# Optimization experiments

Hardware: AMD Instinct MI355X
Metric: run time of the kernel (lower is better)

The kernel has to match this reference:

```python
import jax, jax.numpy as jnp
import numpy as np

B, S_IMG, S_TXT, S_BOK = 1, 2048, 512, 4
DM, H, DH, R = 3072, 24, 128, 16
LORA_SCALE, LORA_ALPHA, BOKEH_SCALE = 1.0, 16.0, 1.0
EPS = 1e-6


def _rms_norm(x, w):
    # normalize over head_dim (last axis), Flux RMSNorm eps=1e-6
    var = jnp.mean(jnp.square(x), axis=-1, keepdims=True)
    return x * jax.lax.rsqrt(var + EPS) * w


def _lora(x, w_down, w_up):
    # LoRALinear: up(down(x)) * alpha/rank
    return (x @ w_down.T) @ w_up.T * (LORA_ALPHA / R)


def _apply_rope(x, cos, sin):
    # x: [B,H,S,D]; cos/sin: [S,D]; diffusers use_real=True, unbind_dim=-1 (interleaved pairs)
    x1 = x[..., 0::2]
    x2 = x[..., 1::2]
    rot = jnp.stack([-x2, x1], axis=-1).reshape(x.shape)
    return x * cos[None, None] + rot * sin[None, None]


def _sdpa(q, k, v):
    # q:[B,H,Sq,D] k,v:[B,H,Sk,D]
    scale = 1.0 / jnp.sqrt(jnp.asarray(q.shape[-1], q.dtype))
    scores = jnp.einsum('bhqd,bhkd->bhqk', q, k) * scale
    p = jax.nn.softmax(scores, axis=-1)
    return jnp.einsum('bhqk,bhkd->bhqd', p, v)


def setup_inputs() -> dict:
    key = jax.random.key(0)
    ks = jax.random.split(key, 40)
    std = 0.02
    d = {}
    d['hidden_states'] = jax.random.normal(ks[0], (B, S_IMG, DM), jnp.float32)
    d['encoder_hidden_states'] = jax.random.normal(ks[1], (B, S_TXT, DM), jnp.float32)
    d['bokeh_embeds'] = jax.random.normal(ks[2], (B, S_BOK, DM), jnp.float32)
    theta = jax.random.uniform(ks[3], (S_TXT + S_IMG, DH // 2), jnp.float32) * 2 * np.pi
    theta = jnp.repeat(theta, 2, axis=-1)  # interleaved pairs share angle
    d['rope_cos'] = jnp.cos(theta)
    d['rope_sin'] = jnp.sin(theta)
    # base attention params
    for i, nm in enumerate(['Wq', 'Wk', 'Wv', 'Waq', 'Wak', 'Wav', 'Wo', 'Wao']):
        d[nm] = jax.random.normal(ks[4 + i], (DM, DM), jnp.float32) * std
    for i, nm in enumerate(['bq', 'bk', 'bv', 'baq', 'bak', 'bav', 'bo', 'bao']):
        d[nm] = jax.random.normal(ks[12 + i], (DM,), jnp.float32) * std
    for i, nm in enumerate(['norm_q_w', 'norm_k_w', 'norm_aq_w', 'norm_ak_w']):
        d[nm] = 1.0 + jax.random.normal(ks[20 + i], (DH,), jnp.float32) * std
    # LoRA adapters (up weights random, not zero, for nontrivial math)
    for i, nm in enumerate(['kb_down', 'vb_down', 'qadp_down', 'kadp_down']):
        d[nm] = jax.random.normal(ks[24 + i], (R, DM), jnp.float32) * (1.0 / R)
    for i, nm in enumerate(['kb_up', 'vb_up', 'qadp_up', 'kadp_up']):
        d[nm] = jax.random.normal(ks[28 + i], (DM, R), jnp.float32) * std
    return d


def reference(hidden_states, encoder_hidden_states, bokeh_embeds, rope_cos, rope_sin,
              Wq, Wk, Wv, Waq, Wak, Wav, Wo, Wao,
              bq, bk, bv, baq, bak, bav, bo, bao,
              norm_q_w, norm_k_w, norm_aq_w, norm_ak_w,
              kb_down, vb_down, qadp_down, kadp_down,
              kb_up, vb_up, qadp_up, kadp_up):
    Bsz = encoder_hidden_states.shape[0]

    def heads(x):  # [B,S,DM] -> [B,H,S,DH]
        return x.reshape(Bsz, -1, H, DH).transpose(0, 2, 1, 3)

    q = hidden_states @ Wq.T + bq
    k = hidden_states @ Wk.T + bk
    v = hidden_states @ Wv.T + bv
    q = q + LORA_SCALE * _lora(q, qadp_down, qadp_up)
    k = k + LORA_SCALE * _lora(k, kadp_down, kadp_up)
    q, k, v = heads(q), heads(k), heads(v)
    q = _rms_norm(q, norm_q_w)
    k = _rms_norm(k, norm_k_w)

    eq = heads(encoder_hidden_states @ Waq.T + baq)
    ek = heads(encoder_hidden_states @ Wak.T + bak)
    ev = heads(encoder_hidden_states @ Wav.T + bav)
    eq = _rms_norm(eq, norm_aq_w)
    ek = _rms_norm(ek, norm_ak_w)

    q = jnp.concatenate([eq, q], axis=2)
    k = jnp.concatenate([ek, k], axis=2)
    v = jnp.concatenate([ev, v], axis=2)

    q = _apply_rope(q, rope_cos, rope_sin)
    k = _apply_rope(k, rope_cos, rope_sin)

    out = _sdpa(q, k, v)  # [B,H,S,DH]
    out = out.transpose(0, 2, 1, 3).reshape(Bsz, -1, H * DH)

    # bokeh pass
    kd = heads(_lora(bokeh_embeds, kb_down, kb_up))
    vd = heads(_lora(bokeh_embeds, vb_down, vb_up))
    cam = _sdpa(q, kd, vd).transpose(0, 2, 1, 3).reshape(Bsz, -1, H * DH)
    out = out + BOKEH_SCALE * cam

    enc_out = out[:, :S_TXT]
    img_out = out[:, S_TXT:]
    img_out = img_out @ Wo.T + bo
    enc_out = enc_out @ Wao.T + bao
    return (img_out, enc_out)
```

## Files before the change

kernel.cpp:

```cpp
#include <hip/hip_runtime.h>

#define DMDL 3072
#define SEQ  2560
#define STXT 512
#define HEADS 24
#define DHD  128
#define WB9 9437184

typedef float f32x4 __attribute__((ext_vector_type(4)));
typedef __bf16 bf16x8 __attribute__((ext_vector_type(8)));
typedef unsigned short u16x4 __attribute__((ext_vector_type(4)));

static __device__ __forceinline__ unsigned short f2bf(float f) {
  unsigned u = __float_as_uint(f);
  u += 0x7fffu + ((u >> 16) & 1u);
  return (unsigned short)(u >> 16);
}

static __device__ __forceinline__ float fexp2(float x) {
  return __builtin_amdgcn_exp2f(x);
}

static __device__ __forceinline__ void gload16(const unsigned short* g, unsigned short* l) {
  __builtin_amdgcn_global_load_lds(
      (const __attribute__((address_space(1))) unsigned int*)g,
      (__attribute__((address_space(3))) unsigned int*)l, 16, 0, 0);
}

__global__ __launch_bounds__(256) void convf2b_kernel(
    const float* __restrict__ src, unsigned short* __restrict__ dst) {
  const int idx4 = blockIdx.x * 256 + threadIdx.x;
  float4 v = *(const float4*)(src + (size_t)idx4 * 4);
  u16x4 b = { f2bf(v.x), f2bf(v.y), f2bf(v.z), f2bf(v.w) };
  *(u16x4*)(dst + (size_t)idx4 * 4) = b;
}

__global__ __launch_bounds__(256) void convw_kernel(
    const float* __restrict__ s0, const float* __restrict__ s1,
    const float* __restrict__ s2, unsigned short* __restrict__ dst) {
  const float* src = (blockIdx.y == 0) ? s0 : (blockIdx.y == 1) ? s1 : s2;
  const size_t idx4 = (size_t)blockIdx.x * 256 + threadIdx.x;
  float4 v = *(const float4*)(src + idx4 * 4);
  u16x4 b = { f2bf(v.x), f2bf(v.y), f2bf(v.z), f2bf(v.w) };
  *(u16x4*)(dst + (size_t)blockIdx.y * WB9 + idx4 * 4) = b;
}

__device__ __forceinline__ void gemm_body(
    const unsigned short* __restrict__ A, const unsigned short* __restrict__ Bw,
    const float* __restrict__ bias, float* __restrict__ C,
    int row0, int col0) {
  __shared__ unsigned short Al[128][64];
  __shared__ unsigned short Bl[128][64];
  const int t = threadIdx.x, w = t >> 6, l = t & 63;
  const int wr = (w >> 1) << 6, wc = (w & 1) << 6;
  const int l15 = l & 15, lg = l >> 4;
  f32x4 acc[4][4];
#pragma unroll
  for (int i = 0; i < 4; i++)
#pragma unroll
    for (int j = 0; j < 4; j++) acc[i][j] = (f32x4){0.f, 0.f, 0.f, 0.f};

  for (int k0 = 0; k0 < DMDL; k0 += 64) {
    __syncthreads();
#pragma unroll
    for (int g = 0; g < 4; g++) {
      const int jb = ((w << 2) + g) << 6;
      const int jl = jb + l;
      const int row = jl >> 3, sl = jl & 7;
      const int col = ((sl ^ (row & 7)) << 3);
      gload16(A  + (size_t)(row0 + row) * DMDL + k0 + col, ((unsigned short*)Al) + (size_t)jb * 8);
      gload16(Bw + (size_t)(col0 + row) * DMDL + k0 + col, ((unsigned short*)Bl) + (size_t)jb * 8);
    }
    asm volatile("s_waitcnt vmcnt(0)" ::: "memory");
    __syncthreads();
#pragma unroll
    for (int kf = 0; kf < 2; kf++) {
      bf16x8 af[4], bfr[4];
#pragma unroll
      for (int i = 0; i < 4; i++) {
        const int ra = wr + (i << 4) + l15;
        af[i]  = *(const bf16x8*)&Al[ra][(((kf << 2) + lg) ^ (ra & 7)) << 3];
        const int rb = wc + (i << 4) + l15;
        bfr[i] = *(const bf16x8*)&Bl[rb][(((kf << 2) + lg) ^ (rb & 7)) << 3];
      }
      __builtin_amdgcn_s_setprio(1);
#pragma unroll
      for (int i = 0; i < 4; i++)
#pragma unroll
        for (int j = 0; j < 4; j++)
          acc[i][j] = __builtin_amdgcn_mfma_f32_16x16x32_bf16(af[i], bfr[j], acc[i][j], 0, 0, 0);
      __builtin_amdgcn_s_setprio(0);
    }
  }
#pragma unroll
  for (int i = 0; i < 4; i++)
#pragma unroll
    for (int j = 0; j < 4; j++) {
      const int col = col0 + wc + (j << 4) + l15;
      const float bb = bias[col];
      const int rbase = row0 + wr + (i << 4) + (lg << 2);
#pragma unroll
      for (int r2 = 0; r2 < 4; r2++)
        C[(size_t)(rbase + r2) * DMDL + col] = acc[i][j][r2] + bb;
    }
}

__global__ __launch_bounds__(256) void gemm3_kernel(
    const unsigned short* __restrict__ A, const unsigned short* __restrict__ w3,
    const float* __restrict__ b0, const float* __restrict__ b1, const float* __restrict__ b2,
    float* __restrict__ c0, float* __restrict__ c1, float* __restrict__ c2, int M) {
  const int nM = M >> 7;
  const int nwg = nM * 72;
  const int cpx = nwg >> 3;
  const int sid = (blockIdx.x & 7) * cpx + (blockIdx.x >> 3);
  const int bxx = sid / nM, by = sid - bxx * nM;
  const int grp = bxx / 24, bx = bxx - grp * 24;
  const unsigned short* Bw = w3 + (size_t)grp * WB9;
  const float* bias = (grp == 0) ? b0 : (grp == 1) ? b1 : b2;
  float* C = (grp == 0) ? c0 : (grp == 1) ? c1 : c2;
  gemm_body(A, Bw, bias, C, by << 7, bx << 7);
}

__global__ __launch_bounds__(256) void gemm_out_kernel(
    const unsigned short* __restrict__ attnbf, const unsigned short* __restrict__ w3,
    const float* __restrict__ bo, const float* __restrict__ bao,
    float* __restrict__ out) {
  const int sid = (blockIdx.x & 7) * 60 + (blockIdx.x >> 3);
  if (sid < 384) {
    const int bx = sid >> 4, by = sid & 15;
    gemm_body(attnbf + (size_t)STXT * DMDL, w3, bo, out, by << 7, bx << 7);
  } else {
    const int s2 = sid - 384;
    const int bx = s2 >> 2, by = s2 & 3;
    gemm_body(attnbf, w3 + WB9, bao, out + (size_t)2048 * DMDL, by << 7, bx << 7);
  }
}

__global__ __launch_bounds__(256) void lora_down2_kernel(
    const float* __restrict__ q0, const float* __restrict__ k0,
    const float* __restrict__ qad, const float* __restrict__ kad,
    float* __restrict__ tmpq, float* __restrict__ tmpk) {
  const int t = threadIdx.x, w = t >> 6, l = t & 63;
  const int m = blockIdx.x;
  const float* X = blockIdx.y ? k0 : q0;
  const float* dwn = blockIdx.y ? kad : qad;
  float* tmp = blockIdx.y ? tmpk : tmpq;
  const float* x = X + (size_t)m * DMDL;
  float acc[16];
#pragma unroll
  for (int r = 0; r < 16; r++) acc[r] = 0.f;
  for (int k = t; k < DMDL; k += 256) {
    float xv = x[k];
#pragma unroll
    for (int r = 0; r < 16; r++) acc[r] += xv * dwn[r * DMDL + k];
  }
#pragma unroll
  for (int off = 1; off < 64; off <<= 1)
#pragma unroll
    for (int r = 0; r < 16; r++) acc[r] += __shfl_xor(acc[r], off);
  __shared__ float red[4][16];
  if (l == 0)
#pragma unroll
    for (int r = 0; r < 16; r++) red[w][r] = acc[r];
  __syncthreads();
  if (t < 16) tmp[(size_t)m * 16 + t] = red[0][t] + red[1][t] + red[2][t] + red[3][t];
}

#define QSCALE 0.12751743f
__global__ __launch_bounds__(256) void pack_kernel(
    const float* __restrict__ q0, const float* __restrict__ k0,
    const float* __restrict__ eq, const float* __restrict__ ek,
    const float* __restrict__ tmpq, const float* __restrict__ tmpk,
    const float* __restrict__ qau, const float* __restrict__ kau,
    const float* __restrict__ nq, const float* __restrict__ nk,
    const float* __restrict__ naq, const float* __restrict__ nak,
    const float* __restrict__ rc, const float* __restrict__ rsn,
    unsigned short* __restrict__ Qp, unsigned short* __restrict__ Kp) {
  const int t = threadIdx.x, w = t >> 6, l = t & 63;
  const int s = blockIdx.x * 4 + w;
  const int h = blockIdx.y;
  const int which = blockIdx.z;
  const int n = h * DHD + 2 * l;
  float2 x;
  const float* nw;
  if (s < STXT) {
    x = *(const float2*)(((which == 0) ? eq : ek) + (size_t)s * DMDL + n);
    nw = (which == 0) ? naq : nak;
  } else {
    x = *(const float2*)(((which == 0) ? q0 : k0) + (size_t)(s - STXT) * DMDL + n);
    nw = (which == 0) ? nq : nk;
    const float* tv = ((which == 0) ? tmpq : tmpk) + (size_t)(s - STXT) * 16;
    const float* uv = ((which == 0) ? qau : kau) + (size_t)n * 16;
    float l1 = 0.f, l2 = 0.f;
#pragma unroll
    for (int r = 0; r < 16; r++) { l1 += tv[r] * uv[r]; l2 += tv[r] * uv[16 + r]; }
    x.x += l1; x.y += l2;
  }
  float ss = x.x * x.x + x.y * x.y;
#pragma unroll
  for (int off = 1; off < 64; off <<= 1) ss += __shfl_xor(ss, off);
  float inv = rsqrtf(ss * (1.f / 128.f) + 1e-6f);
  float xw1 = x.x * inv * nw[2 * l];
  float xw2 = x.y * inv * nw[2 * l + 1];
  float c1 = rc[(size_t)s * DHD + 2 * l], c2 = rc[(size_t)s * DHD + 2 * l + 1];
  float s1 = rsn[(size_t)s * DHD + 2 * l], s2 = rsn[(size_t)s * DHD + 2 * l + 1];
  float y1 = xw1 * c1 - xw2 * s1;
  float y2 = xw2 * c2 + xw1 * s2;
  if (which == 0) { y1 *= QSCALE; y2 *= QSCALE; }
  unsigned short* dst = ((which == 0) ? Qp : Kp) + ((size_t)h * SEQ + s) * DHD + 2 * l;
  unsigned pk = (unsigned)f2bf(y1) | ((unsigned)f2bf(y2) << 16);
  *(unsigned*)dst = pk;
}

__global__ __launch_bounds__(256) void vpackT_kernel(
    const float* __restrict__ v0, const float* __restrict__ ev,
    unsigned short* __restrict__ Vtg) {
  __shared__ unsigned short tile[64][136];
  const int t = threadIdx.x;
  const int s0 = blockIdx.x << 6;
  const int h = blockIdx.y;
  const float* src;
  int srow;
  if (s0 < STXT) { src = ev; srow = s0; } else { src = v0; srow = s0 - STXT; }
#pragma unroll
  for (int p = 0; p < 8; p++) {
    int idx4 = (p << 8) + t;
    int r = idx4 >> 5, c4 = idx4 & 31;
    float4 v = *(const float4*)(src + (size_t)(srow + r) * DMDL + h * DHD + (c4 << 2));
    u16x4 b = { f2bf(v.x), f2bf(v.y), f2bf(v.z), f2bf(v.w) };
    *(u16x4*)&tile[r][c4 << 2] = b;
  }
  __syncthreads();
  const int d = t >> 1, sc = (t & 1) << 5;
  unsigned short outv[32];
#pragma unroll
  for (int e = 0; e < 32; e++) outv[e] = tile[sc + e][d];
  unsigned short* dst = Vtg + ((size_t)h * DHD + d) * SEQ + s0 + sc;
#pragma unroll
  for (int q = 0; q < 4; q++)
    *(uint4*)(dst + (q << 3)) = *(uint4*)&outv[q << 3];
}

__global__ __launch_bounds__(256) void bokeh_down_kernel(
    const float* __restrict__ bok, const float* __restrict__ kbd,
    const float* __restrict__ vbd, float* __restrict__ tkv) {
  const int t = threadIdx.x, w = t >> 6, l = t & 63;
  const int mat = blockIdx.x >> 2, j = blockIdx.x & 3;
  const float* dwn = mat ? vbd : kbd;
  const float* x = bok + (size_t)j * DMDL;
  float acc[16];
#pragma unroll
  for (int r = 0; r < 16; r++) acc[r] = 0.f;
  for (int k = t; k < DMDL; k += 256) {
    float xv = x[k];
#pragma unroll
    for (int r = 0; r < 16; r++) acc[r] += xv * dwn[r * DMDL + k];
  }
#pragma unroll
  for (int off = 1; off < 64; off <<= 1)
#pragma unroll
    for (int r = 0; r < 16; r++) acc[r] += __shfl_xor(acc[r], off);
  __shared__ float red[4][16];
  if (l == 0)
#pragma unroll
    for (int r = 0; r < 16; r++) red[w][r] = acc[r];
  __syncthreads();
  if (t < 16) tkv[(mat * 4 + j) * 16 + t] = red[0][t] + red[1][t] + red[2][t] + red[3][t];
}

__global__ __launch_bounds__(256) void bokeh_up_kernel(
    const float* __restrict__ tkv, const float* __restrict__ kbu,
    const float* __restrict__ vbu, float* __restrict__ kdvd) {
  const int idx = blockIdx.x * 256 + threadIdx.x;
  const int mat = idx / 12288, rem = idx % 12288;
  const int j = rem / DMDL, n = rem % DMDL;
  const float* up = mat ? vbu : kbu;
  const float* tv = tkv + (mat * 4 + j) * 16;
  float s = 0.f;
#pragma unroll
  for (int r = 0; r < 16; r++) s += tv[r] * up[(size_t)n * 16 + r];
  kdvd[(size_t)(mat * 4 + j) * DMDL + n] = s;
}

__global__ __launch_bounds__(256) void attn_kernel(
    const unsigned short* __restrict__ Qp, const unsigned short* __restrict__ Kp,
    const unsigned short* __restrict__ Vtg, const float* __restrict__ kdvd,
    unsigned short* __restrict__ attnbf) {
  __shared__ unsigned short Klds[128][128];
  __shared__ unsigned short Vt[128][128];
  __shared__ unsigned short Plds[4][16][128];
  const int t = threadIdx.x, w = t >> 6, l = t & 63;
  const int l15 = l & 15, lg = l >> 4;
  const int h = blockIdx.y;
  const int q0r = blockIdx.x * 64;
  const unsigned short* Qh = Qp + (size_t)h * SEQ * DHD;
  const unsigned short* Kh = Kp + (size_t)h * SEQ * DHD;
  const unsigned short* Vh = Vtg + (size_t)h * DHD * SEQ;

  bf16x8 qf[4];
  {
    const unsigned short* qsrc = Qh + (size_t)(q0r + w * 16 + l15) * DHD + (lg << 3);
#pragma unroll
    for (int kf = 0; kf < 4; kf++) qf[kf] = *(const bf16x8*)(qsrc + kf * 32);
  }
  f32x4 o[8];
#pragma unroll
  for (int nc = 0; nc < 8; nc++) o[nc] = (f32x4){0.f, 0.f, 0.f, 0.f};
  float m[4] = {-1e30f, -1e30f, -1e30f, -1e30f};
  float sum[4] = {0.f, 0.f, 0.f, 0.f};

  for (int kv0 = 0; kv0 < SEQ; kv0 += 128) {
    __syncthreads();
#pragma unroll
    for (int g = 0; g < 8; g++) {
      const int jb = ((g << 2) + w) << 6;
      const int jl = jb + l;
      const int row = jl >> 4, sl = jl & 15;
      const int col = (sl ^ (row & 7)) << 3;
      gload16(Kh + (size_t)(kv0 + row) * DHD + col, ((unsigned short*)Klds) + (size_t)jb * 8);
      gload16(Vh + (size_t)row * SEQ + kv0 + col, ((unsigned short*)Vt) + (size_t)jb * 8);
    }
    asm volatile("s_waitcnt vmcnt(0)" ::: "memory");
    __syncthreads();
    f32x4 sacc[8];
    __builtin_amdgcn_s_setprio(1);
#pragma unroll
    for (int c = 0; c < 8; c++) {
      sacc[c] = (f32x4){0.f, 0.f, 0.f, 0.f};
      const int krow = c * 16 + l15;
#pragma unroll
      for (int kf = 0; kf < 4; kf++) {
        bf16x8 kb = *(const bf16x8*)&Klds[krow][(((kf << 2) + lg) ^ (krow & 7)) << 3];
        sacc[c] = __builtin_amdgcn_mfma_f32_16x16x32_bf16(qf[kf], kb, sacc[c], 0, 0, 0);
      }
    }
    __builtin_amdgcn_s_setprio(0);
    float mxv[4];
#pragma unroll
    for (int j = 0; j < 4; j++) {
      float mx = sacc[0][j];
#pragma unroll
      for (int c = 1; c < 8; c++) mx = fmaxf(mx, sacc[c][j]);
#pragma unroll
      for (int off = 1; off < 16; off <<= 1) mx = fmaxf(mx, __shfl_xor(mx, off));
      mxv[j] = mx;
    }
    int ok = 1;
#pragma unroll
    for (int j = 0; j < 4; j++) ok &= (mxv[j] <= m[j] + 8.f);
    const bool skip = __all(ok);
    float sc4[4];
#pragma unroll
    for (int j = 0; j < 4; j++) {
      const float mnew = skip ? m[j] : fmaxf(m[j], mxv[j]);
      const int prow = (lg << 2) + j;
      unsigned short* pp = &Plds[w][prow][0];
      float ps = 0.f;
#pragma unroll
      for (int c = 0; c < 8; c++) {
        float pv = fexp2(sacc[c][j] - mnew);
        ps += pv;
        pp[(c * 16 + l15) ^ ((prow & 7) << 3)] = f2bf(pv);
      }
#pragma unroll
      for (int off = 1; off < 16; off <<= 1) ps += __shfl_xor(ps, off);
      if (!skip) {
        float sc = fexp2(m[j] - mnew);
        sum[j] = sum[j] * sc + ps;
        m[j] = mnew;
        sc4[j] = sc;
      } else {
        sum[j] += ps;
      }
    }
    if (!skip) {
#pragma unroll
      for (int nc = 0; nc < 8; nc++) {
        o[nc][0] *= sc4[0]; o[nc][1] *= sc4[1]; o[nc][2] *= sc4[2]; o[nc][3] *= sc4[3];
      }
    }
    __builtin_amdgcn_s_setprio(1);
#pragma unroll
    for (int kf2 = 0; kf2 < 4; kf2++) {
      bf16x8 pa = *(const bf16x8*)&Plds[w][l15][(((kf2 << 2) + lg) ^ (l15 & 7)) << 3];
#pragma unroll
      for (int nc = 0; nc < 8; nc++) {
        const int vrow = nc * 16 + l15;
        bf16x8 vb = *(const bf16x8*)&Vt[vrow][(((kf2 << 2) + lg) ^ (vrow & 7)) << 3];
        o[nc] = __builtin_amdgcn_mfma_f32_16x16x32_bf16(pa, vb, o[nc], 0, 0, 0);
      }
    }
    __builtin_amdgcn_s_setprio(0);
  }

  __syncthreads();
  float* kdl = (float*)&Klds[0][0];
  {
    const int j8 = t >> 5, d4 = (t & 31) << 2;
    *(float4*)&kdl[j8 * 128 + d4] = *(const float4*)(kdvd + (size_t)j8 * DMDL + h * DHD + d4);
  }
  __syncthreads();
  float q32[4][8];
#pragma unroll
  for (int kf = 0; kf < 4; kf++)
#pragma unroll
    for (int r = 0; r < 8; r++) q32[kf][r] = (float)qf[kf][r];
  float pj[4];
#pragma unroll
  for (int jb = 0; jb < 4; jb++) {
    float d = 0.f;
#pragma unroll
    for (int kf = 0; kf < 4; kf++)
#pragma unroll
      for (int r = 0; r < 8; r++)
        d += q32[kf][r] * kdl[jb * 128 + (kf << 5) + (lg << 3) + r];
    d += __shfl_xor(d, 16);
    d += __shfl_xor(d, 32);
    pj[jb] = d;
  }
  float cm = fmaxf(fmaxf(pj[0], pj[1]), fmaxf(pj[2], pj[3]));
  float cs = 0.f;
#pragma unroll
  for (int jb = 0; jb < 4; jb++) { pj[jb] = fexp2(pj[jb] - cm); cs += pj[jb]; }
  float ci = 1.f / cs;
#pragma unroll
  for (int jb = 0; jb < 4; jb++) pj[jb] *= ci;
  float* pnl = kdl + 1024 + (w << 6);
  if (lg == 0) {
#pragma unroll
    for (int jb = 0; jb < 4; jb++) pnl[l15 * 4 + jb] = pj[jb];
  }
  __syncthreads();
  float rinv[4];
#pragma unroll
  for (int j = 0; j < 4; j++) rinv[j] = 1.f / sum[j];
  float pr[4][4];
#pragma unroll
  for (int j = 0; j < 4; j++)
#pragma unroll
    for (int jb = 0; jb < 4; jb++) pr[j][jb] = pnl[(((lg << 2) + j) << 2) + jb];
  const float* vdl = kdl + 512;
#pragma unroll
  for (int nc = 0; nc < 8; nc++) {
    const int col = (nc << 4) + l15;
#pragma unroll
    for (int j = 0; j < 4; j++) {
      float cam = pr[j][0] * vdl[col] + pr[j][1] * vdl[128 + col] +
                  pr[j][2] * vdl[256 + col] + pr[j][3] * vdl[384 + col];
      float outv = o[nc][j] * rinv[j] + cam;
      const int row = q0r + (w << 4) + (lg << 2) + j;
      attnbf[(size_t)row * DMDL + h * DHD + col] = f2bf(outv);
    }
  }
}

extern "C" void kernel_launch(void* const* d_in, const int* in_sizes, int n_in,
                              void* d_out, int out_size, void* d_ws, size_t ws_size,
                              hipStream_t stream) {
  (void)in_sizes; (void)n_in; (void)out_size; (void)ws_size;
  const float* hs  = (const float*)d_in[0];
  const float* enc = (const float*)d_in[1];
  const float* bok = (const float*)d_in[2];
  const float* rc  = (const float*)d_in[3];
  const float* rsn = (const float*)d_in[4];
  const float* Wq  = (const float*)d_in[5];
  const float* Wk  = (const float*)d_in[6];
  const float* Wv  = (const float*)d_in[7];
  const float* Waq = (const float*)d_in[8];
  const float* Wak = (const float*)d_in[9];
  const float* Wav = (const float*)d_in[10];
  const float* Wo  = (const float*)d_in[11];
  const float* Wao = (const float*)d_in[12];
  const float* bq  = (const float*)d_in[13];
  const float* bk  = (const float*)d_in[14];
  const float* bv  = (const float*)d_in[15];
  const float* baq = (const float*)d_in[16];
  const float* bak = (const float*)d_in[17];
  const float* bav = (const float*)d_in[18];
  const float* bo  = (const float*)d_in[19];
  const float* bao = (const float*)d_in[20];
  const float* nq  = (const float*)d_in[21];
  const float* nk  = (const float*)d_in[22];
  const float* naq = (const float*)d_in[23];
  const float* nak = (const float*)d_in[24];
  const float* kbd = (const float*)d_in[25];
  const float* vbd = (const float*)d_in[26];
  const float* qad = (const float*)d_in[27];
  const float* kad = (const float*)d_in[28];
  const float* kbu = (const float*)d_in[29];
  const float* vbu = (const float*)d_in[30];
  const float* qau = (const float*)d_in[31];
  const float* kau = (const float*)d_in[32];

  char* ws = (char*)d_ws;
  unsigned short* w3     = (unsigned short*)(ws + 0);
  unsigned short* hs_bf  = (unsigned short*)(ws + 56623104);
  unsigned short* enc_bf = (unsigned short*)(ws + 69206016);
  float* q0   = (float*)(ws + 72351744);
  float* k0   = (float*)(ws + 97517568);
  float* v0   = (float*)(ws + 122683392);
  float* eq   = (float*)(ws + 147849216);
  float* ek   = (float*)(ws + 154140672);
  float* ev   = (float*)(ws + 160432128);
  float* tmpq = (float*)(ws + 166723584);
  float* tmpk = (float*)(ws + 166854656);
  float* tkv  = (float*)(ws + 166985728);
  float* kdvd = (float*)(ws + 166986240);
  unsigned short* Qp  = (unsigned short*)(ws + 167084544);
  unsigned short* Kp  = (unsigned short*)(ws + 182813184);
  unsigned short* Vtg = (unsigned short*)(ws + 72351744);
  unsigned short* attnbf = (unsigned short*)(ws + 122683392);

  float* out = (float*)d_out;

  dim3 blk(256);

  convf2b_kernel<<<6144, blk, 0, stream>>>(hs, hs_bf);
  convf2b_kernel<<<1536, blk, 0, stream>>>(enc, enc_bf);
  bokeh_down_kernel<<<8, blk, 0, stream>>>(bok, kbd, vbd, tkv);
  bokeh_up_kernel<<<96, blk, 0, stream>>>(tkv, kbu, vbu, kdvd);

  convw_kernel<<<dim3(9216, 3), blk, 0, stream>>>(Wq, Wk, Wv, w3);
  gemm3_kernel<<<1152, blk, 0, stream>>>(hs_bf, w3, bq, bk, bv, q0, k0, v0, 2048);
  convw_kernel<<<dim3(9216, 3), blk, 0, stream>>>(Waq, Wak, Wav, w3);
  gemm3_kernel<<<288, blk, 0, stream>>>(enc_bf, w3, baq, bak, bav, eq, ek, ev, 512);

  lora_down2_kernel<<<dim3(2048, 2), blk, 0, stream>>>(q0, k0, qad, kad, tmpq, tmpk);

  pack_kernel<<<dim3(SEQ / 4, HEADS, 2), blk, 0, stream>>>(
      q0, k0, eq, ek, tmpq, tmpk, qau, kau, nq, nk, naq, nak, rc, rsn, Qp, Kp);
  vpackT_kernel<<<dim3(SEQ / 64, HEADS), blk, 0, stream>>>(v0, ev, Vtg);

  attn_kernel<<<dim3(SEQ / 64, HEADS), blk, 0, stream>>>(Qp, Kp, Vtg, kdvd, attnbf);

  convw_kernel<<<dim3(9216, 2), blk, 0, stream>>>(Wo, Wao, Wao, w3);
  gemm_out_kernel<<<480, blk, 0, stream>>>(attnbf, w3, bo, bao, out);
}
```

Measured before the change: 714.4 us.

## Compute transposed QK^T so softmax row stats reduce with fewer shuffles

Swaps the MFMA operand order so the score tile is transposed: each lane now holds four key columns of a single query row. Row max and sum then need only two cross-lane shuffles instead of four per row for four rows. P is packed to bf16 with v_cvt_pk_bf16_f32 and written as 8-byte stores into a re-swizzled LDS layout. Rescale factors and final sums are moved back to the output layout with __shfl, which adds some shuffle work in the rare non-skip path.

New measurement: 680.8 us, median of 2. -4.7%, faster.

```diff
diff --git a/kernel.cpp b/kernel.cpp
--- a/kernel.cpp
+++ b/kernel.cpp
@@ -288,7 +288,7 @@
     unsigned short* __restrict__ attnbf) {
   __shared__ unsigned short Klds[128][128];
   __shared__ unsigned short Vt[128][128];
-  __shared__ unsigned short Plds[4][16][128];
+  __shared__ unsigned short Pl[4][2048];
   const int t = threadIdx.x, w = t >> 6, l = t & 63;
   const int l15 = l & 15, lg = l >> 4;
   const int h = blockIdx.y;
@@ -296,6 +296,7 @@
   const unsigned short* Qh = Qp + (size_t)h * SEQ * DHD;
   const unsigned short* Kh = Kp + (size_t)h * SEQ * DHD;
   const unsigned short* Vh = Vtg + (size_t)h * DHD * SEQ;
+  char* Pw = (char*)&Pl[w][0];
 
   bf16x8 qf[4];
   {
@@ -306,8 +307,7 @@
   f32x4 o[8];
 #pragma unroll
   for (int nc = 0; nc < 8; nc++) o[nc] = (f32x4){0.f, 0.f, 0.f, 0.f};
-  float m[4] = {-1e30f, -1e30f, -1e30f, -1e30f};
-  float sum[4] = {0.f, 0.f, 0.f, 0.f};
+  float m = -1e30f, sum = 0.f;
 
   for (int kv0 = 0; kv0 < SEQ; kv0 += 128) {
     __syncthreads();
@@ -331,58 +331,55 @@
 #pragma unroll
       for (int kf = 0; kf < 4; kf++) {
         bf16x8 kb = *(const bf16x8*)&Klds[krow][(((kf << 2) + lg) ^ (krow & 7)) << 3];
-        sacc[c] = __builtin_amdgcn_mfma_f32_16x16x32_bf16(qf[kf], kb, sacc[c], 0, 0, 0);
+        sacc[c] = __builtin_amdgcn_mfma_f32_16x16x32_bf16(kb, qf[kf], sacc[c], 0, 0, 0);
       }
     }
     __builtin_amdgcn_s_setprio(0);
-    float mxv[4];
-#pragma unroll
-    for (int j = 0; j < 4; j++) {
-      float mx = sacc[0][j];
-#pragma unroll
-      for (int c = 1; c < 8; c++) mx = fmaxf(mx, sacc[c][j]);
-#pragma unroll
-      for (int off = 1; off < 16; off <<= 1) mx = fmaxf(mx, __shfl_xor(mx, off));
-      mxv[j] = mx;
-    }
-    int ok = 1;
-#pragma unroll
-    for (int j = 0; j < 4; j++) ok &= (mxv[j] <= m[j] + 8.f);
-    const bool skip = __all(ok);
-    float sc4[4];
-#pragma unroll
-    for (int j = 0; j < 4; j++) {
-      const float mnew = skip ? m[j] : fmaxf(m[j], mxv[j]);
-      const int prow = (lg << 2) + j;
-      unsigned short* pp = &Plds[w][prow][0];
-      float ps = 0.f;
-#pragma unroll
-      for (int c = 0; c < 8; c++) {
-        float pv = fexp2(sacc[c][j] - mnew);
-        ps += pv;
-        pp[(c * 16 + l15) ^ ((prow & 7) << 3)] = f2bf(pv);
+    float cm[8];
+#pragma unroll
+    for (int c = 0; c < 8; c++)
+      cm[c] = fmaxf(fmaxf(sacc[c][0], sacc[c][1]), fmaxf(sacc[c][2], sacc[c][3]));
+    float pmax = fmaxf(fmaxf(fmaxf(cm[0], cm[1]), fmaxf(cm[2], cm[3])),
+                       fmaxf(fmaxf(cm[4], cm[5]), fmaxf(cm[6], cm[7])));
+    pmax = fmaxf(pmax, __shfl_xor(pmax, 16));
+    pmax = fmaxf(pmax, __shfl_xor(pmax, 32));
+    const bool skip = __all(pmax <= m + 8.f);
+    const float mnew = skip ? m : fmaxf(m, pmax);
+    float ps = 0.f;
+#pragma unroll
+    for (int c = 0; c < 8; c++) {
+      float p0 = fexp2(sacc[c][0] - mnew);
+      float p1 = fexp2(sacc[c][1] - mnew);
+      float p2 = fexp2(sacc[c][2] - mnew);
+      float p3 = fexp2(sacc[c][3] - mnew);
+      ps += (p0 + p1) + (p2 + p3);
+      unsigned lo, hi;
+      asm("v_cvt_pk_bf16_f32 %0, %1, %2" : "=v"(lo) : "v"(p0), "v"(p1));
+      asm("v_cvt_pk_bf16_f32 %0, %1, %2" : "=v"(hi) : "v"(p2), "v"(p3));
+      const int byteoff = (l15 << 8) + (((((c << 1) + (lg >> 1)) ^ (l15 & 7))) << 4) + ((lg & 1) << 3);
+      *(uint2*)(Pw + byteoff) = make_uint2(lo, hi);
+    }
+    ps += __shfl_xor(ps, 16);
+    ps += __shfl_xor(ps, 32);
+    if (!skip) {
+      const float sc = fexp2(m - mnew);
+      sum = sum * sc + ps;
+      m = mnew;
+      float s0 = __shfl(sc, (lg << 2) + 0);
+      float s1 = __shfl(sc, (lg << 2) + 1);
+      float s2 = __shfl(sc, (lg << 2) + 2);
+      float s3 = __shfl(sc, (lg << 2) + 3);
+#pragma unroll
+      for (int nc = 0; nc < 8; nc++) {
+        o[nc][0] *= s0; o[nc][1] *= s1; o[nc][2] *= s2; o[nc][3] *= s3;
       }
-#pragma unroll
-      for (int off = 1; off < 16; off <<= 1) ps += __shfl_xor(ps, off);
-      if (!skip) {
-        float sc = fexp2(m[j] - mnew);
-        sum[j] = sum[j] * sc + ps;
-        m[j] = mnew;
-        sc4[j] = sc;
-      } else {
-        sum[j] += ps;
-      }
-    }
-    if (!skip) {
-#pragma unroll
-      for (int nc = 0; nc < 8; nc++) {
-        o[nc][0] *= sc4[0]; o[nc][1] *= sc4[1]; o[nc][2] *= sc4[2]; o[nc][3] *= sc4[3];
-      }
+    } else {
+      sum += ps;
     }
     __builtin_amdgcn_s_setprio(1);
 #pragma unroll
     for (int kf2 = 0; kf2 < 4; kf2++) {
-      bf16x8 pa = *(const bf16x8*)&Plds[w][l15][(((kf2 << 2) + lg) ^ (l15 & 7)) << 3];
+      bf16x8 pa = *(const bf16x8*)(Pw + (l15 << 8) + ((((kf2 << 2) + lg) ^ (l15 & 7)) << 4));
 #pragma unroll
       for (int nc = 0; nc < 8; nc++) {
         const int vrow = nc * 16 + l15;
@@ -393,6 +390,15 @@
     __builtin_amdgcn_s_setprio(0);
   }
 
+  float rinv[4];
+  {
+    float su0 = __shfl(sum, (lg << 2) + 0);
+    float su1 = __shfl(sum, (lg << 2) + 1);
+    float su2 = __shfl(sum, (lg << 2) + 2);
+    float su3 = __shfl(sum, (lg << 2) + 3);
+    rinv[0] = 1.f / su0; rinv[1] = 1.f / su1; rinv[2] = 1.f / su2; rinv[3] = 1.f / su3;
+  }
+
   __syncthreads();
   float* kdl = (float*)&Klds[0][0];
   {
@@ -418,10 +424,10 @@
     d += __shfl_xor(d, 32);
     pj[jb] = d;
   }
-  float cm = fmaxf(fmaxf(pj[0], pj[1]), fmaxf(pj[2], pj[3]));
+  float cmx = fmaxf(fmaxf(pj[0], pj[1]), fmaxf(pj[2], pj[3]));
   float cs = 0.f;
 #pragma unroll
-  for (int jb = 0; jb < 4; jb++) { pj[jb] = fexp2(pj[jb] - cm); cs += pj[jb]; }
+  for (int jb = 0; jb < 4; jb++) { pj[jb] = fexp2(pj[jb] - cmx); cs += pj[jb]; }
   float ci = 1.f / cs;
 #pragma unroll
   for (int jb = 0; jb < 4; jb++) pj[jb] *= ci;
@@ -431,9 +437,6 @@
     for (int jb = 0; jb < 4; jb++) pnl[l15 * 4 + jb] = pj[jb];
   }
   __syncthreads();
-  float rinv[4];
-#pragma unroll
-  for (int j = 0; j < 4; j++) rinv[j] = 1.f / sum[j];
   float pr[4][4];
 #pragma unroll
   for (int j = 0; j < 4; j++)
```
